# Optimization experiments

Measured on AMD Instinct MI355X. Metric: run time of the kernel, lower is better.

## Reference

```python
import jax, jax.numpy as jnp
import numpy as np

B, L, E, D, H, P, NL = 4, 2048, 7, 512, 8, 720, 2
DH = D // H
FACTOR = 5
U = min(L, FACTOR * int(np.ceil(np.log(L))))  # top-u queries, = 40
SCALE = 1.0 / np.sqrt(DH)


def setup_inputs() -> dict:
    key = jax.random.key(0)
    ks = jax.random.split(key, 12)
    s = 0.02
    rn = lambda k, shape: jax.random.normal(k, shape, jnp.float32) * s
    return {
        "x": jax.random.normal(ks[0], (B, L, E), jnp.float32),
        "emb_w": rn(ks[1], (E, D)), "emb_b": jnp.zeros((D,), jnp.float32),
        "Wq": rn(ks[2], (NL, D, D)), "bq": jnp.zeros((NL, D), jnp.float32),
        "Wk": rn(ks[3], (NL, D, D)), "bk": jnp.zeros((NL, D), jnp.float32),
        "Wv": rn(ks[4], (NL, D, D)), "bv": jnp.zeros((NL, D), jnp.float32),
        "Wo": rn(ks[5], (NL, D, D)), "bo": jnp.zeros((NL, D), jnp.float32),
        "W1": rn(ks[6], (NL, D, D)), "b1": jnp.zeros((NL, D), jnp.float32),
        "W2": rn(ks[7], (NL, D, D)), "b2": jnp.zeros((NL, D), jnp.float32),
        "ln1_g": jnp.ones((NL, D), jnp.float32), "ln1_b": jnp.zeros((NL, D), jnp.float32),
        "ln2_g": jnp.ones((NL, D), jnp.float32), "ln2_b": jnp.zeros((NL, D), jnp.float32),
        "proj_w": rn(ks[8], (D, E)), "proj_b": jnp.zeros((E,), jnp.float32),
    }


def layer_norm(x, g, b):
    m = jnp.mean(x, axis=-1, keepdims=True)
    v = jnp.mean(jnp.square(x - m), axis=-1, keepdims=True)
    return (x - m) * jax.lax.rsqrt(v + 1e-5) * g + b


def prob_sparse_attn(x, Wq, bq, Wk, bk, Wv, bv, Wo, bo):
    # x: [B, L, D] -> heads [B, H, L, DH]
    q = (x @ Wq + bq).reshape(B, L, H, DH).transpose(0, 2, 1, 3)
    k = (x @ Wk + bk).reshape(B, L, H, DH).transpose(0, 2, 1, 3)
    v = (x @ Wv + bv).reshape(B, L, H, DH).transpose(0, 2, 1, 3)
    scores = jnp.einsum('bhqd,bhkd->bhqk', q, k) * SCALE  # [B,H,L,L]
    # sparsity measure M(q) = max_k - mean_k
    M = jnp.max(scores, axis=-1) - jnp.mean(scores, axis=-1)  # [B,H,L]
    _, idx = jax.lax.top_k(M, U)  # [B,H,U] indices of active queries
    s_top = jnp.take_along_axis(scores, idx[..., None], axis=2)  # [B,H,U,L]
    attn = jax.nn.softmax(s_top, axis=-1)
    upd = jnp.einsum('bhul,bhld->bhud', attn, v)  # [B,H,U,DH]
    # lazy queries get the mean of V; active queries get attention output
    ctx = jnp.broadcast_to(jnp.mean(v, axis=2, keepdims=True), v.shape)
    bidx = jnp.arange(B)[:, None, None]
    hidx = jnp.arange(H)[None, :, None]
    ctx = ctx.at[bidx, hidx, idx].set(upd)  # scatter active queries
    out = ctx.transpose(0, 2, 1, 3).reshape(B, L, D)
    return out @ Wo + bo


def reference(x, emb_w, emb_b, Wq, bq, Wk, bk, Wv, bv, Wo, bo,
              W1, b1, W2, b2, ln1_g, ln1_b, ln2_g, ln2_b, proj_w, proj_b):
    h = x @ emb_w + emb_b  # [B,L,D]
    for i in range(NL):
        a = prob_sparse_attn(h, Wq[i], bq[i], Wk[i], bk[i], Wv[i], bv[i], Wo[i], bo[i])
        h = layer_norm(h + a, ln1_g[i], ln1_b[i])
        f = jax.nn.relu(h @ W1[i] + b1[i]) @ W2[i] + b2[i]
        h = layer_norm(h + f, ln2_g[i], ln2_b[i])
    return h[:, -P:, :] @ proj_w + proj_b  # [B,P,E]
```

## Files before the change

### kernel.cpp

```cpp
#include <hip/hip_runtime.h>
#include <hip/hip_bf16.h>
#include <cstdint>
#include <cstddef>

#define BB 4
#define LL 2048
#define EE 7
#define DD 512
#define HH 8
#define DHH 64
#define PP 720
#define NLAYER 2
#define UU 40
#define SCALE 0.125f
#define ROWS (BB*LL)
#define BIGN ((size_t)ROWS*DD)
#define NIN 21
#define FCH 256
#define NCH (LL/FCH)
#define PSTR 264
#define VSTR 136
#define WOFF 1280
#define WTPB 12
#define WRPB 768

typedef unsigned short u16;
typedef unsigned long long u64;
typedef __bf16 bf16x8 __attribute__((ext_vector_type(8)));
typedef float  f32x4  __attribute__((ext_vector_type(4)));

__device__ __forceinline__ float bf2f(u16 u){
  union { uint32_t i; float f; } c; c.i = ((uint32_t)u) << 16; return c.f;
}
__device__ __forceinline__ u16 f2b(float f){
  __hip_bfloat16 h = __float2bfloat16(f);
  return *(u16*)&h;
}
__device__ __forceinline__ void gld_lds16(const u16* g, u16* l){
  __builtin_amdgcn_global_load_lds(
      (const __attribute__((address_space(1))) uint32_t*)g,
      (__attribute__((address_space(3))) uint32_t*)l, 16, 0, 0);
}
__device__ __forceinline__ int is_bf16(const void* d15){
  return (*(const uint32_t*)d15 == 0x3F800000u) ? 0 : 1;
}

__device__ __forceinline__ void addln_row_vals(const u16* a, const u16* r,
    const float* g, const float* bvec, int row, int lane, u16 ob[8]){
  size_t base = (size_t)row * DD + lane*8;
  ushort4 a0 = *(const ushort4*)(a + base);
  ushort4 a1 = *(const ushort4*)(a + base + 4);
  ushort4 r0 = *(const ushort4*)(r + base);
  ushort4 r1 = *(const ushort4*)(r + base + 4);
  float x[8] = {bf2f(a0.x)+bf2f(r0.x), bf2f(a0.y)+bf2f(r0.y),
                bf2f(a0.z)+bf2f(r0.z), bf2f(a0.w)+bf2f(r0.w),
                bf2f(a1.x)+bf2f(r1.x), bf2f(a1.y)+bf2f(r1.y),
                bf2f(a1.z)+bf2f(r1.z), bf2f(a1.w)+bf2f(r1.w)};
  float s = 0.f;
  #pragma unroll
  for (int i=0;i<8;i++) s += x[i];
  #pragma unroll
  for (int off=1; off<64; off<<=1) s += __shfl_xor(s, off);
  float mean = s * (1.0f/DD);
  float vs = 0.f;
  #pragma unroll
  for (int i=0;i<8;i++){ x[i] -= mean; vs += x[i]*x[i]; }
  #pragma unroll
  for (int off=1; off<64; off<<=1) vs += __shfl_xor(vs, off);
  float rs = rsqrtf(vs * (1.0f/DD) + 1e-5f);
  const float* gp = g + lane*8;
  const float* bp = bvec + lane*8;
  #pragma unroll
  for (int i=0;i<8;i++) ob[i] = f2b(x[i]*rs*gp[i] + bp[i]);
}

__device__ __forceinline__ void tile_map(int flat, int tilesPerB, int winOff,
                                         int* mbRow, int* nbOut){
  int mq = tilesPerB >> 1;
  int xcd = flat & 7, rest = flat >> 3;
  int mbi = xcd + 8*(rest % mq);
  int bat = mbi / tilesPerB;
  *mbRow = bat*LL + winOff + (mbi - bat*tilesPerB)*64;
  *nbOut = (rest / mq) * 128;
}

#define NSMALL 15
struct ConvArgs { const void* src[NSMALL]; int off[NSMALL]; int n[NSMALL]; };
struct WPtrs { const void* p[6]; };

__global__ __launch_bounds__(256) void k_preamble(ConvArgs a, WPtrs wp,
    const void* __restrict__ xraw, const void* __restrict__ d15,
    float* __restrict__ dst, float* __restrict__ zbuf,
    u16* __restrict__ hB, u16* __restrict__ wT){
  int y = blockIdx.y, bx = blockIdx.x, t = threadIdx.x;
  int isbf = is_bf16(d15);
  __shared__ u16 tile[64][65];
  __shared__ float xs[32][EE];
  if (y < NSMALL){
    int i = bx*256 + t;
    if (i >= a.n[y]) return;
    float v;
    if (isbf) v = bf2f(((const u16*)a.src[y])[i]);
    else      v = ((const float*)a.src[y])[i];
    dst[(size_t)a.off[y] + i] = v;
  } else if (y == NSMALL){
    int i = bx*256 + t;
    if (i < NLAYER*4096) zbuf[i] = 0.f;
  } else if (y < 32){
    int flat = (y - 16)*256 + bx;
    if (flat >= 512) return;
    int colgrp = flat & 1;
    int rowbase = (flat >> 1) * 32;
    int dd = colgrp*256 + t;
    if (t < 32*EE){
      int j = t / EE, e = t - j*EE;
      xs[j][e] = isbf ? bf2f(((const u16*)xraw)[(rowbase + j)*EE + e])
                      : ((const float*)xraw)[(rowbase + j)*EE + e];
    }
    float wreg[EE];
    #pragma unroll
    for (int e=0;e<EE;e++)
      wreg[e] = isbf ? bf2f(((const u16*)a.src[1])[e*DD + dd])
                     : ((const float*)a.src[1])[e*DD + dd];
    float bias = isbf ? bf2f(((const u16*)a.src[2])[dd]) : ((const float*)a.src[2])[dd];
    __syncthreads();
    for (int j=0;j<32;j++){
      float acc = bias;
      #pragma unroll
      for (int e=0;e<EE;e++) acc = fmaf(xs[j][e], wreg[e], acc);
      hB[(size_t)(rowbase + j)*DD + dd] = f2b(acc);
    }
  } else {
    int flat = (y - 32)*256 + bx;
    int mz = flat >> 6, tl = flat & 63;
    int lay = mz / 6, mat = mz % 6;
    int n0 = (tl & 7)*64, k0 = (tl >> 3)*64;
    int r = t >> 6, c = t & 63;
    const void* src = wp.p[mat];
    for (int rr = r; rr < 64; rr += 4){
      size_t idx = ((size_t)lay*DD + (k0+rr))*DD + n0 + c;
      u16 v;
      if (isbf) v = ((const u16*)src)[idx];
      else      v = f2b(((const float*)src)[idx]);
      tile[rr][c] = v;
    }
    __syncthreads();
    u16* drow = wT + ((size_t)mz*DD + n0)*DD + k0;
    int c4 = (t & 15)*4;
    for (int rr = (t >> 4); rr < 64; rr += 16){
      ushort4 v = { tile[c4][rr], tile[c4+1][rr], tile[c4+2][rr], tile[c4+3][rr] };
      *(ushort4*)(drow + (size_t)rr*DD + c4) = v;
    }
  }
}

__global__ __launch_bounds__(256) void k_gemm_mfma(const u16* __restrict__ A, const u16* __restrict__ Bt,
    const float* __restrict__ bias, u16* __restrict__ Cb, int relu,
    int tilesPerB, int winOff){
  __shared__ u16 As[64*64];
  __shared__ u16 Bs[128*64];
  int t = threadIdx.x, wave = t >> 6, lane = t & 63;
  int qlane = lane & 15, quad = lane >> 4;
  int flat = blockIdx.x + gridDim.x*blockIdx.y;
  int mb, nb;
  tile_map(flat, tilesPerB, winOff, &mb, &nb);
  int wm = (wave & 1) * 32, wn = (wave >> 1) * 64;
  f32x4 acc[2][4];
  #pragma unroll
  for (int i=0;i<2;i++)
    #pragma unroll
    for (int j=0;j<4;j++) acc[i][j] = (f32x4){0.f,0.f,0.f,0.f};

  int srow = wave*8 + (lane>>3);
  int scol = (((lane&7) ^ ((lane>>3)&7))) * 8;
  const u16* Ag = A + (size_t)(mb + srow)*DD + scol;
  const u16* Bg = Bt + (size_t)(nb + srow)*DD + scol;

  for (int k0 = 0; k0 < DD; k0 += 64){
    __syncthreads();
    #pragma unroll
    for (int i=0;i<2;i++)
      gld_lds16(Ag + (size_t)i*32*DD + k0, As + (i*32 + wave*8)*64);
    #pragma unroll
    for (int i=0;i<4;i++)
      gld_lds16(Bg + (size_t)i*32*DD + k0, Bs + (i*32 + wave*8)*64);
    __syncthreads();
    #pragma unroll
    for (int ch=0; ch<2; ++ch){
      bf16x8 af[2], bfv[4];
      int cgL = ((ch*4 + quad) ^ (qlane & 7)) * 8;
      #pragma unroll
      for (int i=0;i<2;i++) af[i] = *(const bf16x8*)(As + (wm + i*16 + qlane)*64 + cgL);
      #pragma unroll
      for (int j=0;j<4;j++) bfv[j] = *(const bf16x8*)(Bs + (wn + j*16 + qlane)*64 + cgL);
      #pragma unroll
      for (int i=0;i<2;i++)
        #pragma unroll
        for (int j=0;j<4;j++)
          acc[i][j] = __builtin_amdgcn_mfma_f32_16x16x32_bf16(af[i], bfv[j], acc[i][j], 0, 0, 0);
    }
  }
  #pragma unroll
  for (int i=0;i<2;i++){
    int rbase = mb + wm + i*16 + quad*4;
    #pragma unroll
    for (int j=0;j<4;j++){
      int col = nb + wn + j*16 + qlane;
      float bv = bias[col];
      #pragma unroll
      for (int r=0;r<4;r++){
        float cv = acc[i][j][r] + bv;
        if (relu) cv = fmaxf(cv, 0.f);
        Cb[(size_t)(rbase + r)*DD + col] = f2b(cv);
      }
    }
  }
}

__global__ __launch_bounds__(256) void k_gemm_wo(const u64* __restrict__ rowPtr, const u16* __restrict__ Bt,
    const float* __restrict__ bias, u16* __restrict__ Cb,
    int tilesPerB, int winOff){
  __shared__ u16 As[64*64];
  __shared__ u16 Bs[128*64];
  int t = threadIdx.x, wave = t >> 6, lane = t & 63;
  int qlane = lane & 15, quad = lane >> 4;
  int flat = blockIdx.x + gridDim.x*blockIdx.y;
  int mb, nb;
  tile_map(flat, tilesPerB, winOff, &mb, &nb);
  int wm = (wave & 1) * 32, wn = (wave >> 1) * 64;
  f32x4 acc[2][4];
  #pragma unroll
  for (int i=0;i<2;i++)
    #pragma unroll
    for (int j=0;j<4;j++) acc[i][j] = (f32x4){0.f,0.f,0.f,0.f};

  int srow = wave*8 + (lane>>3);
  int scol = (((lane&7) ^ ((lane>>3)&7))) * 8;
  const u16* Bg = Bt + (size_t)(nb + srow)*DD + scol;

  for (int k0 = 0; k0 < DD; k0 += 64){
    int slice = k0 >> 6;
    __syncthreads();
    #pragma unroll
    for (int i=0;i<2;i++){
      int arow = mb + i*32 + srow;
      const u16* src = (const u16*)(uintptr_t)rowPtr[(size_t)arow*8 + slice] + scol;
      gld_lds16(src, As + (i*32 + wave*8)*64);
    }
    #pragma unroll
    for (int i=0;i<4;i++)
      gld_lds16(Bg + (size_t)i*32*DD + k0, Bs + (i*32 + wave*8)*64);
    __syncthreads();
    #pragma unroll
    for (int ch=0; ch<2; ++ch){
      bf16x8 af[2], bfv[4];
      int cgL = ((ch*4 + quad) ^ (qlane & 7)) * 8;
      #pragma unroll
      for (int i=0;i<2;i++) af[i] = *(const bf16x8*)(As + (wm + i*16 + qlane)*64 + cgL);
      #pragma unroll
      for (int j=0;j<4;j++) bfv[j] = *(const bf16x8*)(Bs + (wn + j*16 + qlane)*64 + cgL);
      #pragma unroll
      for (int i=0;i<2;i++)
        #pragma unroll
        for (int j=0;j<4;j++)
          acc[i][j] = __builtin_amdgcn_mfma_f32_16x16x32_bf16(af[i], bfv[j], acc[i][j], 0, 0, 0);
    }
  }
  #pragma unroll
  for (int i=0;i<2;i++){
    int rbase = mb + wm + i*16 + quad*4;
    #pragma unroll
    for (int j=0;j<4;j++){
      int col = nb + wn + j*16 + qlane;
      float bv = bias[col];
      #pragma unroll
      for (int r=0;r<4;r++){
        float cv = acc[i][j][r] + bv;
        Cb[(size_t)(rbase + r)*DD + col] = f2b(cv);
      }
    }
  }
}

__global__ __launch_bounds__(256) void k_gemm_qkv(const u16* __restrict__ A, const u16* __restrict__ Wt,
    const float* __restrict__ bq, const float* __restrict__ bk, const float* __restrict__ bv,
    u16* __restrict__ qB, u16* __restrict__ kB, u16* __restrict__ vB,
    float* __restrict__ ksum, float* __restrict__ vsum){
  __shared__ u16 As[128*64];
  __shared__ u16 Bs[3][64*64];
  int t = threadIdx.x, wave = t >> 6, lane = t & 63;
  int qlane = lane & 15, quad = lane >> 4;
  int flat = blockIdx.x + gridDim.x*blockIdx.y;
  int xcd = flat & 7, rest = flat >> 3;
  int mb  = (xcd + 8*(rest & 7)) * 128;
  int nb  = (rest >> 3) * 64;
  int wm  = wave * 32;
  f32x4 acc[3][2][4];
  #pragma unroll
  for (int s=0;s<3;s++)
    #pragma unroll
    for (int i=0;i<2;i++)
      #pragma unroll
      for (int j=0;j<4;j++) acc[s][i][j] = (f32x4){0.f,0.f,0.f,0.f};

  int srow = wave*8 + (lane>>3);
  int scol = (((lane&7) ^ ((lane>>3)&7))) * 8;
  const u16* Ag = A + (size_t)(mb + srow)*DD + scol;
  const u16* Bg = Wt + (size_t)(nb + srow)*DD + scol;

  for (int k0 = 0; k0 < DD; k0 += 64){
    __syncthreads();
    #pragma unroll
    for (int i=0;i<4;i++)
      gld_lds16(Ag + (size_t)i*32*DD + k0, As + (i*32 + wave*8)*64);
    #pragma unroll
    for (int s=0;s<3;s++)
      #pragma unroll
      for (int i=0;i<2;i++)
        gld_lds16(Bg + (size_t)s*DD*DD + (size_t)i*32*DD + k0, Bs[s] + (i*32 + wave*8)*64);
    __syncthreads();
    #pragma unroll
    for (int ch=0; ch<2; ++ch){
      int cgL = ((ch*4 + quad) ^ (qlane & 7)) * 8;
      bf16x8 af[2];
      #pragma unroll
      for (int i=0;i<2;i++) af[i] = *(const bf16x8*)(As + (wm + i*16 + qlane)*64 + cgL);
      #pragma unroll
      for (int s=0;s<3;s++){
        bf16x8 bf[4];
        #pragma unroll
        for (int j=0;j<4;j++) bf[j] = *(const bf16x8*)(Bs[s] + (j*16 + qlane)*64 + cgL);
        #pragma unroll
        for (int i=0;i<2;i++)
          #pragma unroll
          for (int j=0;j<4;j++)
            acc[s][i][j] = __builtin_amdgcn_mfma_f32_16x16x32_bf16(af[i], bf[j], acc[s][i][j], 0, 0, 0);
      }
    }
  }
  #pragma unroll
  for (int s=0;s<3;s++){
    const float* bias = (s==0) ? bq : (s==1) ? bk : bv;
    u16* out = (s==0) ? qB : (s==1) ? kB : vB;
    float csum[4] = {0.f,0.f,0.f,0.f};
    #pragma unroll
    for (int j=0;j<4;j++){
      int col = nb + j*16 + qlane;
      float bvv = bias[col];
      #pragma unroll
      for (int i=0;i<2;i++){
        int rbase = mb + wm + i*16 + quad*4;
        #pragma unroll
        for (int r=0;r<4;r++){
          float cv = acc[s][i][j][r] + bvv;
          out[(size_t)(rbase + r)*DD + col] = f2b(cv);
          csum[j] += cv;
        }
      }
    }
    if (s > 0){
      float* dst = (s==1) ? ksum : vsum;
      int bidx = mb >> 11;
      #pragma unroll
      for (int j=0;j<4;j++){
        float v = csum[j];
        v += __shfl_xor(v, 16);
        v += __shfl_xor(v, 32);
        if ((lane>>4) == 0)
          atomicAdd(dst + bidx*512 + nb + j*16 + lane, v);
      }
    }
  }
}

__global__ __launch_bounds__(256) void k_sparsity_mfma(const u16* __restrict__ qB, const u16* __restrict__ kB,
    const float* __restrict__ ksum, float* __restrict__ Mout){
  int flat = blockIdx.x + gridDim.x*blockIdx.y;
  int xcd = flat & 7, rest = flat >> 3;
  int qc = rest & 15;
  int bh = (rest >> 4)*8 + xcd;
  int b = bh >> 3, hh = bh & 7;
  int q0 = qc * 128;
  int t = threadIdx.x, wave = t >> 6, lane = t & 63;
  const u16* qbase = qB + ((size_t)(b*LL + q0))*DD + hh*DHH;
  const u16* kbase = kB + ((size_t)b*LL)*DD + hh*DHH;
  bf16x8 qa[8][2];
  #pragma unroll
  for (int i=0;i<8;i++)
    #pragma unroll
    for (int c=0;c<2;c++)
      qa[i][c] = *(const bf16x8*)(qbase + (size_t)(i*16 + (lane&15))*DD + c*32 + (lane>>4)*8);
  float rmax[8][4];
  #pragma unroll
  for (int i=0;i<8;i++)
    #pragma unroll
    for (int r=0;r<4;r++) rmax[i][r] = -3.0e38f;
  for (int kt = wave*16; kt < LL; kt += 64){
    bf16x8 kb0 = *(const bf16x8*)(kbase + (size_t)(kt + (lane&15))*DD + (lane>>4)*8);
    bf16x8 kb1 = *(const bf16x8*)(kbase + (size_t)(kt + (lane&15))*DD + 32 + (lane>>4)*8);
    #pragma unroll
    for (int i=0;i<8;i++){
      f32x4 a = (f32x4){0.f,0.f,0.f,0.f};
      a = __builtin_amdgcn_mfma_f32_16x16x32_bf16(qa[i][0], kb0, a, 0, 0, 0);
      a = __builtin_amdgcn_mfma_f32_16x16x32_bf16(qa[i][1], kb1, a, 0, 0, 0);
      #pragma unroll
      for (int r=0;r<4;r++) rmax[i][r] = fmaxf(rmax[i][r], a[r]);
    }
  }
  #pragma unroll
  for (int i=0;i<8;i++)
    #pragma unroll
    for (int r=0;r<4;r++){
      float v = rmax[i][r];
      v = fmaxf(v, __shfl_xor(v, 1));
      v = fmaxf(v, __shfl_xor(v, 2));
      v = fmaxf(v, __shfl_xor(v, 4));
      v = fmaxf(v, __shfl_xor(v, 8));
      rmax[i][r] = v;
    }
  __shared__ float smax[4][128];
  if ((lane & 15) == 0){
    #pragma unroll
    for (int i=0;i<8;i++)
      #pragma unroll
      for (int r=0;r<4;r++)
        smax[wave][i*16 + (lane>>4)*4 + r] = rmax[i][r];
  }
  __syncthreads();
  if (t < 128){
    float mx = fmaxf(fmaxf(smax[0][t], smax[1][t]), fmaxf(smax[2][t], smax[3][t]));
    const u16* qrow = qB + (size_t)(b*LL + q0 + t)*DD + hh*DHH;
    float dot = 0.f;
    #pragma unroll
    for (int dv=0; dv<16; ++dv){
      ushort4 qv = *(const ushort4*)(qrow + dv*4);
      const float* kp = ksum + bh*DHH + dv*4;
      dot += bf2f(qv.x)*kp[0] + bf2f(qv.y)*kp[1]
           + bf2f(qv.z)*kp[2] + bf2f(qv.w)*kp[3];
    }
    Mout[bh*LL + q0 + t] = SCALE * (mx - dot * (1.0f/LL));
  }
}

__global__ __launch_bounds__(256) void k_flash(const u16* __restrict__ qB, const u16* __restrict__ kB,
    const u16* __restrict__ vB, const float* __restrict__ Mv, int* __restrict__ sidx,
    float* __restrict__ pO, float* __restrict__ pM, float* __restrict__ pS){
  int bh = blockIdx.y, c = blockIdx.x;
  int b = bh >> 3, hh = bh & 7;
  int t = threadIdx.x, w = t >> 6, lane = t & 63;
  int qlane = lane & 15, quad = lane >> 4;
  int l0 = c * FCH;
  __shared__ u16 Ps[48*PSTR];
  __shared__ union { uint32_t keys[LL]; u16 vst[64*VSTR]; } uu;
  __shared__ float wred[4][48];
  __shared__ float mrow[48];
  __shared__ int hist[256];
  __shared__ int scr[2];
  __shared__ int tieIdx[64];
  __shared__ int counters[2];
  __shared__ int sidxL[UU], sidxS[UU];

  {
    const float* src = Mv + (size_t)bh*LL;
    #pragma unroll
    for (int j = 0; j < 8; ++j){
      int idx = t + j*256;
      uint32_t u = __float_as_uint(src[idx]);
      uu.keys[idx] = (u & 0x80000000u) ? ~u : (u | 0x80000000u);
    }
    uint32_t prefix = 0, pmask = 0;
    int need = UU;
    #pragma unroll
    for (int pass = 0; pass < 4; ++pass){
      int shift = 24 - pass*8;
      __syncthreads();
      hist[t] = 0;
      __syncthreads();
      #pragma unroll
      for (int j = 0; j < 8; ++j){
        uint32_t k = uu.keys[t + j*256];
        if ((k & pmask) == prefix)
          atomicAdd(&hist[(k >> shift) & 0xFF], 1);
      }
      __syncthreads();
      if (t < 64){
        int ln = t;
        int h0 = hist[ln*4+0], h1 = hist[ln*4+1], h2 = hist[ln*4+2], h3 = hist[ln*4+3];
        int s = h0 + h1 + h2 + h3;
        int acc = s;
        #pragma unroll
        for (int off = 1; off < 64; off <<= 1){
          int v = __shfl_down(acc, off);
          if (ln + off < 64) acc += v;
        }
        int c3 = acc - s;
        int c2 = c3 + h3;
        int c1 = c2 + h2;
        int c0 = c1 + h1;
        if      (need > c3 && need <= c3 + h3){ scr[0] = ln*4+3; scr[1] = c3; }
        else if (need > c2 && need <= c2 + h2){ scr[0] = ln*4+2; scr[1] = c2; }
        else if (need > c1 && need <= c1 + h1){ scr[0] = ln*4+1; scr[1] = c1; }
        else if (need > c0 && need <= c0 + h0){ scr[0] = ln*4+0; scr[1] = c0; }
      }
      __syncthreads();
      prefix |= ((uint32_t)scr[0]) << shift;
      need -= scr[1];
      pmask |= 0xFFu << shift;
    }
    if (t < 2) counters[t] = 0;
    __syncthreads();
    uint32_t Tkey = prefix;
    #pragma unroll
    for (int j = 0; j < 8; ++j){
      int idx = t + j*256;
      uint32_t k = uu.keys[idx];
      if (k > Tkey){
        int p = atomicAdd(&counters[0], 1);
        sidxL[p] = idx;
      } else if (k == Tkey){
        int p = atomicAdd(&counters[1], 1);
        if (p < 64) tieIdx[p] = idx;
      }
    }
    __syncthreads();
    if (t == 0){
      int c_gt = counters[0];
      int tc = counters[1];
      int needTies = UU - c_gt;
      if (tc <= 64){
        for (int m = 0; m < needTies; ++m){
          int bestv = 0x7FFFFFFF, bestp = -1;
          for (int q = 0; q < tc; ++q)
            if (tieIdx[q] < bestv){ bestv = tieIdx[q]; bestp = q; }
          sidxL[c_gt + m] = bestv;
          tieIdx[bestp] = 0x7FFFFFFF;
        }
      } else {
        int m = 0;
        for (int j = 0; j < LL && m < needTies; ++j)
          if (uu.keys[j] == Tkey){ sidxL[c_gt + m] = j; m++; }
      }
    }
    __syncthreads();
    int vv = 0, rk = 0;
    if (t < UU){
      vv = sidxL[t];
      #pragma unroll 8
      for (int j = 0; j < UU; ++j) rk += (sidxL[j] < vv) ? 1 : 0;
    }
    __syncthreads();
    if (t < UU) sidxS[rk] = vv;
    __syncthreads();
    if (c == 0 && t < UU) sidx[bh*UU + t] = sidxS[t];
  }

  const u16* kbase = kB + (size_t)b*LL*DD + hh*DHH;
  const u16* vbase = vB + (size_t)b*LL*DD + hh*DHH;
  const u16* qbase = qB + (size_t)b*LL*DD + hh*DHH;

  bf16x8 qa[3][2];
  #pragma unroll
  for (int i=0;i<3;i++){
    int u = i*16 + qlane;
    if (u < UU){
      const u16* qr = qbase + (size_t)sidxS[u]*DD + quad*8;
      qa[i][0] = *(const bf16x8*)qr;
      qa[i][1] = *(const bf16x8*)(qr + 32);
    } else {
      bf16x8 z;
      #pragma unroll
      for (int q8=0;q8<8;q8++) z[q8] = (__bf16)0.0f;
      qa[i][0] = z; qa[i][1] = z;
    }
  }
  f32x4 S[3][4];
  #pragma unroll
  for (int j=0;j<4;j++){
    const u16* kr = kbase + (size_t)(l0 + w*64 + j*16 + qlane)*DD + quad*8;
    bf16x8 k0 = *(const bf16x8*)kr;
    bf16x8 k1 = *(const bf16x8*)(kr + 32);
    #pragma unroll
    for (int i=0;i<3;i++){
      f32x4 a = (f32x4){0.f,0.f,0.f,0.f};
      a = __builtin_amdgcn_mfma_f32_16x16x32_bf16(qa[i][0], k0, a, 0, 0, 0);
      a = __builtin_amdgcn_mfma_f32_16x16x32_bf16(qa[i][1], k1, a, 0, 0, 0);
      S[i][j] = a;
    }
  }
  #pragma unroll
  for (int i=0;i<3;i++){
    #pragma unroll
    for (int r=0;r<4;r++){
      float m = -3.0e38f;
      #pragma unroll
      for (int j=0;j<4;j++){ S[i][j][r] *= SCALE; m = fmaxf(m, S[i][j][r]); }
      m = fmaxf(m, __shfl_xor(m, 1));
      m = fmaxf(m, __shfl_xor(m, 2));
      m = fmaxf(m, __shfl_xor(m, 4));
      m = fmaxf(m, __shfl_xor(m, 8));
      if (qlane == 0) wred[w][i*16 + quad*4 + r] = m;
    }
  }
  __syncthreads();
  if (t < 48) mrow[t] = fmaxf(fmaxf(wred[0][t], wred[1][t]), fmaxf(wred[2][t], wred[3][t]));
  __syncthreads();
  #pragma unroll
  for (int i=0;i<3;i++){
    #pragma unroll
    for (int r=0;r<4;r++){
      int row = i*16 + quad*4 + r;
      float m = mrow[row];
      float ls = 0.f;
      #pragma unroll
      for (int j=0;j<4;j++){
        float e = __expf(S[i][j][r] - m);
        ls += e;
        Ps[row*PSTR + w*64 + j*16 + qlane] = f2b(e);
      }
      ls += __shfl_xor(ls, 1);
      ls += __shfl_xor(ls, 2);
      ls += __shfl_xor(ls, 4);
      ls += __shfl_xor(ls, 8);
      if (qlane == 0) wred[w][row] = ls;
    }
  }
  __syncthreads();
  if (t < 48){
    pM[(bh*NCH + c)*48 + t] = mrow[t];
    pS[(bh*NCH + c)*48 + t] = wred[0][t] + wred[1][t] + wred[2][t] + wred[3][t];
  }
  f32x4 O[3];
  #pragma unroll
  for (int i=0;i<3;i++) O[i] = (f32x4){0.f,0.f,0.f,0.f};
  for (int half = 0; half < 2; ++half){
    __syncthreads();
    for (int idx = t; idx < 128*8; idx += 256){
      int rr = idx >> 3, d8 = idx & 7;
      const u16* src = vbase + (size_t)(l0 + half*128 + rr)*DD + d8*8;
      ushort4 v0 = *(const ushort4*)src;
      ushort4 v1 = *(const ushort4*)(src + 4);
      int d = d8*8;
      uu.vst[(d+0)*VSTR + rr] = v0.x; uu.vst[(d+1)*VSTR + rr] = v0.y;
      uu.vst[(d+2)*VSTR + rr] = v0.z; uu.vst[(d+3)*VSTR + rr] = v0.w;
      uu.vst[(d+4)*VSTR + rr] = v1.x; uu.vst[(d+5)*VSTR + rr] = v1.y;
      uu.vst[(d+6)*VSTR + rr] = v1.z; uu.vst[(d+7)*VSTR + rr] = v1.w;
    }
    __syncthreads();
    #pragma unroll
    for (int ks = 0; ks < 4; ++ks){
      int kloc = half*128 + ks*32;
      bf16x8 bfv = *(const bf16x8*)(uu.vst + (w*16 + qlane)*VSTR + ks*32 + quad*8);
      #pragma unroll
      for (int i=0;i<3;i++){
        bf16x8 af = *(const bf16x8*)(Ps + (i*16 + qlane)*PSTR + kloc + quad*8);
        O[i] = __builtin_amdgcn_mfma_f32_16x16x32_bf16(af, bfv, O[i], 0, 0, 0);
      }
    }
  }
  size_t ob = (size_t)(bh*NCH + c)*48*64;
  #pragma unroll
  for (int i=0;i<3;i++)
    #pragma unroll
    for (int r=0;r<4;r++)
      pO[ob + (size_t)(i*16 + quad*4 + r)*64 + w*16 + qlane] = O[i][r];
}

__global__ __launch_bounds__(256) void k_flash_red(const float* __restrict__ pO, const float* __restrict__ pM,
    const float* __restrict__ pS, const int* __restrict__ sidx, const float* __restrict__ vsum,
    u16* __restrict__ attnC, u16* __restrict__ vmeanB, u64* __restrict__ rowPtr){
  int bh = blockIdx.x; int b = bh >> 3, hh = bh & 7;
  int t = threadIdx.x;
  if (t < 64) vmeanB[b*512 + hh*64 + t] = f2b(vsum[b*512 + hh*64 + t] * (1.0f/LL));
  u64 vmPtr = (u64)(uintptr_t)(vmeanB + b*512 + hh*64);
  for (int row = t; row < LL; row += 256)
    rowPtr[((size_t)b*LL + row)*8 + hh] = vmPtr;
  __syncthreads();
  if (t < UU)
    rowPtr[((size_t)b*LL + sidx[bh*UU + t])*8 + hh] =
        (u64)(uintptr_t)(attnC + ((size_t)bh*UU + t)*64);
  for (int idx = t; idx < UU*64; idx += 256){
    int u = idx >> 6, n = idx & 63;
    float m = -3.0e38f;
    #pragma unroll
    for (int c=0;c<NCH;c++) m = fmaxf(m, pM[(bh*NCH + c)*48 + u]);
    float s = 0.f, o = 0.f;
    #pragma unroll
    for (int c=0;c<NCH;c++){
      float wgt = __expf(pM[(bh*NCH + c)*48 + u] - m);
      s += wgt * pS[(bh*NCH + c)*48 + u];
      o += wgt * pO[((size_t)(bh*NCH + c)*48 + u)*64 + n];
    }
    attnC[((size_t)bh*UU + u)*64 + n] = f2b(o / s);
  }
}

__global__ __launch_bounds__(256) void k_addln(const u16* __restrict__ a, const u16* __restrict__ r,
    const float* __restrict__ g, const float* __restrict__ bvec, u16* __restrict__ outB,
    int rowsPerB, int winOff){
  int g0 = blockIdx.x*4 + (threadIdx.x >> 6);
  int lane = threadIdx.x & 63;
  int bat = g0 / rowsPerB;
  int row = bat*LL + winOff + (g0 - bat*rowsPerB);
  u16 ob[8];
  addln_row_vals(a, r, g, bvec, row, lane, ob);
  size_t base = (size_t)row * DD + lane*8;
  *(ushort4*)(outB + base)     = (ushort4){ob[0],ob[1],ob[2],ob[3]};
  *(ushort4*)(outB + base + 4) = (ushort4){ob[4],ob[5],ob[6],ob[7]};
}

__global__ __launch_bounds__(256) void k_proj_ln(const u16* __restrict__ hIn, const u16* __restrict__ res,
    const float* __restrict__ lng, const float* __restrict__ lnbv,
    const float* __restrict__ pw, const float* __restrict__ pb,
    void* __restrict__ out, const void* __restrict__ d15){
  int w = threadIdx.x >> 6, lane = threadIdx.x & 63;
  int rp = blockIdx.x*4 + w;
  int b = rp / PP, pp = rp - b*PP;
  int row = b*LL + (LL-PP) + pp;
  u16 ob[8];
  addln_row_vals(hIn, res, lng, lnbv, row, lane, ob);
  float x[8];
  #pragma unroll
  for (int j=0;j<8;j++) x[j] = bf2f(ob[j]);
  float acc[EE];
  #pragma unroll
  for (int e=0;e<EE;e++) acc[e]=0.f;
  #pragma unroll
  for (int j=0;j<8;j++){
    const float* wrow = pw + (size_t)(lane*8 + j)*EE;
    #pragma unroll
    for (int e=0;e<EE;e++) acc[e] = fmaf(x[j], wrow[e], acc[e]);
  }
  int isbf = is_bf16(d15);
  #pragma unroll
  for (int e=0;e<EE;e++){
    float rr = acc[e];
    #pragma unroll
    for (int off=32; off>0; off>>=1) rr += __shfl_down(rr, off);
    if (lane == 0){
      float val = rr + pb[e];
      if (isbf) ((__hip_bfloat16*)out)[(size_t)rp*EE + e] = __float2bfloat16(val);
      else      ((float*)out)[(size_t)rp*EE + e] = val;
    }
  }
}

extern "C" void kernel_launch(void* const* d_in, const int* in_sizes, int n_in,
                              void* d_out, int out_size, void* d_ws, size_t ws_size,
                              hipStream_t stream){
  float* ws    = (float*)d_ws;
  float* Mv    = ws;
  float* ksumL = Mv + (size_t)BB*HH*LL;
  float* pM    = ksumL + NLAYER*4096;
  float* pS    = pM + 12288;
  float* pO    = pS + 12288;
  int*   sidx  = (int*)(pO + 786432);
  u64*   rowPtr= (u64*)(((uintptr_t)(sidx + 1280) + 15) & ~(uintptr_t)15);
  u16*   attnC = (u16*)(rowPtr + (size_t)ROWS*8);
  u16*   vmeanB= attnC + (size_t)BB*HH*UU*64;
  u16*   hB    = vmeanB + 2048;
  u16*   qB    = hB + BIGN;
  u16*   kB    = qB + BIGN;
  u16*   vB    = kB + BIGN;
  u16*   f1B   = vB + BIGN;
  u16*   tmpB  = f1B + BIGN;
  u16*   wT    = tmpB + BIGN;
  float* conv  = (float*)(((uintptr_t)(wT + (size_t)12*DD*DD) + 15) & ~(uintptr_t)15);

  static const int small_ids[NSMALL] = {0,1,2,4,6,8,10,12,14,15,16,17,18,19,20};
  ConvArgs ca;
  int off_all[NIN];
  int tot = 0;
  for (int i = 0; i < NIN; ++i) off_all[i] = -1;
  for (int s = 0; s < NSMALL; ++s){
    int i = small_ids[s];
    ca.src[s] = d_in[i];
    ca.off[s] = tot;
    ca.n[s]   = in_sizes[i];
    off_all[i] = tot;
    tot += in_sizes[i];
  }
  const float* bq = conv + off_all[4];
  const float* bk = conv + off_all[6];
  const float* bv = conv + off_all[8];
  const float* bo = conv + off_all[10];
  const float* b1 = conv + off_all[12];
  const float* b2 = conv + off_all[14];
  const float* ln1g = conv + off_all[15]; const float* ln1b = conv + off_all[16];
  const float* ln2g = conv + off_all[17]; const float* ln2b = conv + off_all[18];
  const float* pw = conv + off_all[19]; const float* pb = conv + off_all[20];

  WPtrs wp;
  wp.p[0]=d_in[3]; wp.p[1]=d_in[5]; wp.p[2]=d_in[7];
  wp.p[3]=d_in[9]; wp.p[4]=d_in[11]; wp.p[5]=d_in[13];

  k_preamble<<<dim3(256, 35), 256, 0, stream>>>(ca, wp, d_in[0], d_in[15],
                                                conv, ksumL, hB, wT);

  dim3 gg0(4, 128);
  dim3 gg1(4, WTPB*BB);
  dim3 gq(8, 64);

  for (int l = 0; l < NLAYER; ++l){
    const u16* WqkvT = wT + (size_t)(l*6 + 0)*DD*DD;
    const u16* WoT   = wT + (size_t)(l*6 + 3)*DD*DD;
    const u16* W1T   = wT + (size_t)(l*6 + 4)*DD*DD;
    const u16* W2T   = wT + (size_t)(l*6 + 5)*DD*DD;
    float* ksum = ksumL + l*4096;
    float* vsum = ksum + 2048;

    k_gemm_qkv<<<gq, 256, 0, stream>>>(hB, WqkvT, bq + l*DD, bk + l*DD, bv + l*DD,
                                       qB, kB, vB, ksum, vsum);
    k_sparsity_mfma<<<dim3(LL/128, BB*HH), 256, 0, stream>>>(qB, kB, ksum, Mv);
    k_flash<<<dim3(NCH, BB*HH), 256, 0, stream>>>(qB, kB, vB, Mv, sidx, pO, pM, pS);
    k_flash_red<<<BB*HH, 256, 0, stream>>>(pO, pM, pS, sidx, vsum, attnC, vmeanB, rowPtr);
    if (l < NLAYER - 1){
      k_gemm_wo<<<gg0, 256, 0, stream>>>(rowPtr, WoT, bo + l*DD, tmpB, 32, 0);
      k_addln<<<ROWS/4, 256, 0, stream>>>(hB, tmpB, ln1g + l*DD, ln1b + l*DD, hB, LL, 0);
      k_gemm_mfma<<<gg0, 256, 0, stream>>>(hB, W1T, b1 + l*DD, f1B, 1, 32, 0);
      k_gemm_mfma<<<gg0, 256, 0, stream>>>(f1B, W2T, b2 + l*DD, tmpB, 0, 32, 0);
      k_addln<<<ROWS/4, 256, 0, stream>>>(hB, tmpB, ln2g + l*DD, ln2b + l*DD, hB, LL, 0);
    } else {
      k_gemm_wo<<<gg1, 256, 0, stream>>>(rowPtr, WoT, bo + l*DD, tmpB, WTPB, WOFF);
      k_addln<<<(WRPB*BB)/4, 256, 0, stream>>>(hB, tmpB, ln1g + l*DD, ln1b + l*DD, hB,
                                               WRPB, WOFF);
      k_gemm_mfma<<<gg1, 256, 0, stream>>>(hB, W1T, b1 + l*DD, f1B, 1, WTPB, WOFF);
      k_gemm_mfma<<<gg1, 256, 0, stream>>>(f1B, W2T, b2 + l*DD, tmpB, 0, WTPB, WOFF);
      k_proj_ln<<<(BB*PP)/4, 256, 0, stream>>>(hB, tmpB, ln2g + l*DD, ln2b + l*DD,
                                               pw, pb, d_out, d_in[15]);
    }
  }
}
```

Measured before the change: 345.3 us.

## Compute Wo projection only for rows touched by active queries plus one lazy row

After: 341.7 us. No clear change (-1.0%).

```diff
diff --git a/kernel.cpp b/kernel.cpp
--- a/kernel.cpp
+++ b/kernel.cpp
@@ -23,6 +23,8 @@
 #define WOFF 1280
 #define WTPB 12
 #define WRPB 768
+#define NDIRTY (HH*UU)
+#define WOCROWS (NDIRTY + 64)
 
 typedef unsigned short u16;
 typedef unsigned long long u64;
@@ -45,13 +47,12 @@
   return (*(const uint32_t*)d15 == 0x3F800000u) ? 0 : 1;
 }
 
-__device__ __forceinline__ void addln_row_vals(const u16* a, const u16* r,
-    const float* g, const float* bvec, int row, int lane, u16 ob[8]){
-  size_t base = (size_t)row * DD + lane*8;
-  ushort4 a0 = *(const ushort4*)(a + base);
-  ushort4 a1 = *(const ushort4*)(a + base + 4);
-  ushort4 r0 = *(const ushort4*)(r + base);
-  ushort4 r1 = *(const ushort4*)(r + base + 4);
+__device__ __forceinline__ void addln_core(const u16* arow, const u16* rrow,
+    const float* g, const float* bvec, int lane, u16 ob[8]){
+  ushort4 a0 = *(const ushort4*)(arow + lane*8);
+  ushort4 a1 = *(const ushort4*)(arow + lane*8 + 4);
+  ushort4 r0 = *(const ushort4*)(rrow + lane*8);
+  ushort4 r1 = *(const ushort4*)(rrow + lane*8 + 4);
   float x[8] = {bf2f(a0.x)+bf2f(r0.x), bf2f(a0.y)+bf2f(r0.y),
                 bf2f(a0.z)+bf2f(r0.z), bf2f(a0.w)+bf2f(r0.w),
                 bf2f(a1.x)+bf2f(r1.x), bf2f(a1.y)+bf2f(r1.y),
@@ -217,16 +218,16 @@
   }
 }
 
-__global__ __launch_bounds__(256) void k_gemm_wo(const u64* __restrict__ rowPtr, const u16* __restrict__ Bt,
-    const float* __restrict__ bias, u16* __restrict__ Cb,
-    int tilesPerB, int winOff){
+__global__ __launch_bounds__(256) void k_gemm_wo_d(const u64* __restrict__ rowPtr,
+    const int* __restrict__ dlist, const u16* __restrict__ vmeanB,
+    const u16* __restrict__ Bt, const float* __restrict__ bias, u16* __restrict__ woC){
   __shared__ u16 As[64*64];
   __shared__ u16 Bs[128*64];
   int t = threadIdx.x, wave = t >> 6, lane = t & 63;
   int qlane = lane & 15, quad = lane >> 4;
-  int flat = blockIdx.x + gridDim.x*blockIdx.y;
-  int mb, nb;
-  tile_map(flat, tilesPerB, winOff, &mb, &nb);
+  int nb = blockIdx.x * 128;
+  int ty = blockIdx.y;
+  int b = ty / 6, tile = ty % 6;
   int wm = (wave & 1) * 32, wn = (wave >> 1) * 64;
   f32x4 acc[2][4];
   #pragma unroll
@@ -238,13 +239,23 @@
   int scol = (((lane&7) ^ ((lane>>3)&7))) * 8;
   const u16* Bg = Bt + (size_t)(nb + srow)*DD + scol;
 
+  int drow[2] = {0,0};
+  if (tile < 5){
+    #pragma unroll
+    for (int i=0;i<2;i++)
+      drow[i] = b*LL + dlist[b*NDIRTY + tile*64 + i*32 + srow];
+  }
+
   for (int k0 = 0; k0 < DD; k0 += 64){
     int slice = k0 >> 6;
     __syncthreads();
     #pragma unroll
     for (int i=0;i<2;i++){
-      int arow = mb + i*32 + srow;
-      const u16* src = (const u16*)(uintptr_t)rowPtr[(size_t)arow*8 + slice] + scol;
+      const u16* src;
+      if (tile < 5)
+        src = (const u16*)(uintptr_t)rowPtr[(size_t)drow[i]*8 + slice] + scol;
+      else
+        src = vmeanB + b*512 + slice*64 + scol;
       gld_lds16(src, As + (i*32 + wave*8)*64);
     }
     #pragma unroll
@@ -268,7 +279,7 @@
   }
   #pragma unroll
   for (int i=0;i<2;i++){
-    int rbase = mb + wm + i*16 + quad*4;
+    int rloc = tile*64 + wm + i*16 + quad*4;
     #pragma unroll
     for (int j=0;j<4;j++){
       int col = nb + wn + j*16 + qlane;
@@ -276,7 +287,7 @@
       #pragma unroll
       for (int r=0;r<4;r++){
         float cv = acc[i][j][r] + bv;
-        Cb[(size_t)(rbase + r)*DD + col] = f2b(cv);
+        woC[((size_t)b*WOCROWS + rloc + r)*DD + col] = f2b(cv);
       }
     }
   }
@@ -667,7 +678,8 @@
 
 __global__ __launch_bounds__(256) void k_flash_red(const float* __restrict__ pO, const float* __restrict__ pM,
     const float* __restrict__ pS, const int* __restrict__ sidx, const float* __restrict__ vsum,
-    u16* __restrict__ attnC, u16* __restrict__ vmeanB, u64* __restrict__ rowPtr){
+    u16* __restrict__ attnC, u16* __restrict__ vmeanB, u64* __restrict__ rowPtr,
+    int* __restrict__ dlist, u64* __restrict__ woSrc, u16* __restrict__ woC){
   int bh = blockIdx.x; int b = bh >> 3, hh = bh & 7;
   int t = threadIdx.x;
   if (t < 64) vmeanB[b*512 + hh*64 + t] = f2b(vsum[b*512 + hh*64 + t] * (1.0f/LL));
@@ -692,6 +704,48 @@
     }
     attnC[((size_t)bh*UU + u)*64 + n] = f2b(o / s);
   }
+  if (hh == 0){
+    __shared__ u16 flag[LL];
+    __shared__ int slist[NDIRTY];
+    __shared__ int cnt;
+    for (int i = t; i < LL; i += 256) flag[i] = 0;
+    if (t == 0) cnt = 0;
+    __syncthreads();
+    for (int i = t; i < NDIRTY; i += 256)
+      flag[sidx[b*NDIRTY + i]] = 1;
+    __syncthreads();
+    u16* lazyRow = woC + ((size_t)b*WOCROWS + NDIRTY)*DD;
+    for (int i = t; i < LL; i += 256){
+      int row = b*LL + i;
+      if (flag[i]){
+        int s = atomicAdd(&cnt, 1);
+        slist[s] = i;
+        woSrc[row] = (u64)(uintptr_t)(woC + ((size_t)b*WOCROWS + s)*DD);
+      } else {
+        woSrc[row] = (u64)(uintptr_t)lazyRow;
+      }
+    }
+    __syncthreads();
+    int c0 = cnt, fill = slist[0];
+    for (int i = c0 + t; i < NDIRTY; i += 256) slist[i] = fill;
+    __syncthreads();
+    for (int i = t; i < NDIRTY; i += 256) dlist[b*NDIRTY + i] = slist[i];
+  }
+}
+
+__global__ __launch_bounds__(256) void k_addln_p(const u16* __restrict__ a, const u64* __restrict__ rSrc,
+    const float* __restrict__ g, const float* __restrict__ bvec, u16* __restrict__ outB,
+    int rowsPerB, int winOff){
+  int g0 = blockIdx.x*4 + (threadIdx.x >> 6);
+  int lane = threadIdx.x & 63;
+  int bat = g0 / rowsPerB;
+  int row = bat*LL + winOff + (g0 - bat*rowsPerB);
+  const u16* rrow = (const u16*)(uintptr_t)rSrc[row];
+  u16 ob[8];
+  addln_core(a + (size_t)row*DD, rrow, g, bvec, lane, ob);
+  size_t base = (size_t)row * DD + lane*8;
+  *(ushort4*)(outB + base)     = (ushort4){ob[0],ob[1],ob[2],ob[3]};
+  *(ushort4*)(outB + base + 4) = (ushort4){ob[4],ob[5],ob[6],ob[7]};
 }
 
 __global__ __launch_bounds__(256) void k_addln(const u16* __restrict__ a, const u16* __restrict__ r,
@@ -702,7 +756,7 @@
   int bat = g0 / rowsPerB;
   int row = bat*LL + winOff + (g0 - bat*rowsPerB);
   u16 ob[8];
-  addln_row_vals(a, r, g, bvec, row, lane, ob);
+  addln_core(a + (size_t)row*DD, r + (size_t)row*DD, g, bvec, lane, ob);
   size_t base = (size_t)row * DD + lane*8;
   *(ushort4*)(outB + base)     = (ushort4){ob[0],ob[1],ob[2],ob[3]};
   *(ushort4*)(outB + base + 4) = (ushort4){ob[4],ob[5],ob[6],ob[7]};
@@ -717,7 +771,7 @@
   int b = rp / PP, pp = rp - b*PP;
   int row = b*LL + (LL-PP) + pp;
   u16 ob[8];
-  addln_row_vals(hIn, res, lng, lnbv, row, lane, ob);
+  addln_core(hIn + (size_t)row*DD, res + (size_t)row*DD, lng, lnbv, lane, ob);
   float x[8];
   #pragma unroll
   for (int j=0;j<8;j++) x[j] = bf2f(ob[j]);
@@ -757,7 +811,10 @@
   u64*   rowPtr= (u64*)(((uintptr_t)(sidx + 1280) + 15) & ~(uintptr_t)15);
   u16*   attnC = (u16*)(rowPtr + (size_t)ROWS*8);
   u16*   vmeanB= attnC + (size_t)BB*HH*UU*64;
-  u16*   hB    = vmeanB + 2048;
+  u16*   woC   = vmeanB + 2048;
+  int*   dlist = (int*)(woC + (size_t)BB*WOCROWS*DD);
+  u64*   woSrc = (u64*)(((uintptr_t)(dlist + BB*NDIRTY) + 15) & ~(uintptr_t)15);
+  u16*   hB    = (u16*)(woSrc + ROWS);
   u16*   qB    = hB + BIGN;
   u16*   kB    = qB + BIGN;
   u16*   vB    = kB + BIGN;
@@ -799,6 +856,7 @@
   dim3 gg0(4, 128);
   dim3 gg1(4, WTPB*BB);
   dim3 gq(8, 64);
+  dim3 gwo(4, 6*BB);
 
   for (int l = 0; l < NLAYER; ++l){
     const u16* WqkvT = wT + (size_t)(l*6 + 0)*DD*DD;
@@ -812,17 +870,17 @@
                                        qB, kB, vB, ksum, vsum);
     k_sparsity_mfma<<<dim3(LL/128, BB*HH), 256, 0, stream>>>(qB, kB, ksum, Mv);
     k_flash<<<dim3(NCH, BB*HH), 256, 0, stream>>>(qB, kB, vB, Mv, sidx, pO, pM, pS);
-    k_flash_red<<<BB*HH, 256, 0, stream>>>(pO, pM, pS, sidx, vsum, attnC, vmeanB, rowPtr);
+    k_flash_red<<<BB*HH, 256, 0, stream>>>(pO, pM, pS, sidx, vsum, attnC, vmeanB, rowPtr,
+                                           dlist, woSrc, woC);
+    k_gemm_wo_d<<<gwo, 256, 0, stream>>>(rowPtr, dlist, vmeanB, WoT, bo + l*DD, woC);
     if (l < NLAYER - 1){
-      k_gemm_wo<<<gg0, 256, 0, stream>>>(rowPtr, WoT, bo + l*DD, tmpB, 32, 0);
-      k_addln<<<ROWS/4, 256, 0, stream>>>(hB, tmpB, ln1g + l*DD, ln1b + l*DD, hB, LL, 0);
+      k_addln_p<<<ROWS/4, 256, 0, stream>>>(hB, woSrc, ln1g + l*DD, ln1b + l*DD, hB, LL, 0);
       k_gemm_mfma<<<gg0, 256, 0, stream>>>(hB, W1T, b1 + l*DD, f1B, 1, 32, 0);
       k_gemm_mfma<<<gg0, 256, 0, stream>>>(f1B, W2T, b2 + l*DD, tmpB, 0, 32, 0);
       k_addln<<<ROWS/4, 256, 0, stream>>>(hB, tmpB, ln2g + l*DD, ln2b + l*DD, hB, LL, 0);
     } else {
-      k_gemm_wo<<<gg1, 256, 0, stream>>>(rowPtr, WoT, bo + l*DD, tmpB, WTPB, WOFF);
-      k_addln<<<(WRPB*BB)/4, 256, 0, stream>>>(hB, tmpB, ln1g + l*DD, ln1b + l*DD, hB,
-                                               WRPB, WOFF);
+      k_addln_p<<<(WRPB*BB)/4, 256, 0, stream>>>(hB, woSrc, ln1g + l*DD, ln1b + l*DD, hB,
+                                                 WRPB, WOFF);
       k_gemm_mfma<<<gg1, 256, 0, stream>>>(hB, W1T, b1 + l*DD, f1B, 1, WTPB, WOFF);
       k_gemm_mfma<<<gg1, 256, 0, stream>>>(f1B, W2T, b2 + l*DD, tmpB, 0, WTPB, WOFF);
       k_proj_ln<<<(BB*PP)/4, 256, 0, stream>>>(hB, tmpB, ln2g + l*DD, ln2b + l*DD,
```
